# Kernel optimization log

Hardware: AMD Instinct MI355X
Metric: run time of the kernel (lower is better)

Reference implementation:

```python
import jax, jax.numpy as jnp
import numpy as np

# Each of the 16 binary logic ops (probabilistic relaxation) is affine in (1, a, b, a*b):
# op(a,b) = c0 + ca*a + cb*b + cab*a*b. Rows indexed by op id 0..15.
COEF = jnp.array([
    [0, 0, 0, 0],   # 0: false
    [0, 0, 0, 1],   # 1: a AND b
    [0, 1, 0, -1],  # 2: a AND NOT b
    [0, 1, 0, 0],   # 3: a
    [0, 0, 1, -1],  # 4: NOT a AND b
    [0, 0, 1, 0],   # 5: b
    [0, 1, 1, -2],  # 6: a XOR b
    [0, 1, 1, -1],  # 7: a OR b
    [1, -1, -1, 1], # 8: NOR
    [1, -1, -1, 2], # 9: XNOR
    [1, 0, -1, 0],  # 10: NOT b
    [1, 0, -1, 1],  # 11: a OR NOT b
    [1, -1, 0, 0],  # 12: NOT a
    [1, -1, 0, 1],  # 13: NOT a OR b
    [1, 0, 0, -1],  # 14: NAND
    [1, 0, 0, 0],   # 15: true
], dtype=jnp.float32)

B, C, H, W = 64, 32, 32, 32
K = 64            # num_kernels
D = 4             # tree_depth
S = 2 ** D        # sample_size = 16
RF, STRIDE, PAD = 5, 1, 0


def _make_indices(rng):
    # Replicates get_kernel_indices: per-kernel random (h,w,c) offsets, tiled over all
    # spatial positions. Returns a_idx, b_idx: [K, P, S, 3] with (h, w, c).
    h_starts = np.arange(0, H + 2 * PAD - RF + 1, STRIDE)
    w_starts = np.arange(0, W + 2 * PAD - RF + 1, STRIDE)
    hg, wg = np.meshgrid(h_starts, w_starts, indexing='ij')
    hg, wg = hg.ravel(), wg.ravel()           # [P]
    a_all, b_all = [], []
    for _ in range(K):
        h_off = rng.integers(0, RF, 2 * S)
        w_off = rng.integers(0, RF, 2 * S)
        c_off = rng.integers(0, C, 2 * S)
        hh = h_off[None, :] + hg[:, None]     # [P, 2S]
        ww = w_off[None, :] + wg[:, None]
        cc = np.broadcast_to(c_off[None, :], hh.shape)
        idx = np.stack([hh, ww, cc], axis=-1) # [P, 2S, 3]
        a_all.append(idx[:, :S])
        b_all.append(idx[:, S:])
    return np.stack(a_all).astype(np.int32), np.stack(b_all).astype(np.int32)


def setup_inputs() -> dict:
    key = jax.random.key(0)
    kx, k0, k1, k2, k3, k4 = jax.random.split(key, 6)
    rng = np.random.default_rng(0)
    a_idx, b_idx = _make_indices(rng)
    return {
        'x': jax.random.uniform(kx, (B, C, H, W), dtype=jnp.float32),
        'w0': jax.random.normal(k0, (16, K, 16), dtype=jnp.float32),
        'w1': jax.random.normal(k1, (8, K, 16), dtype=jnp.float32),
        'w2': jax.random.normal(k2, (4, K, 16), dtype=jnp.float32),
        'w3': jax.random.normal(k3, (2, K, 16), dtype=jnp.float32),
        'w4': jax.random.normal(k4, (1, K, 16), dtype=jnp.float32),
        'a_idx': jnp.asarray(a_idx),
        'b_idx': jnp.asarray(b_idx),
    }


def _bin_op(a, b, w):
    # a, b: [B, K, P, L]; w: [L, K, 16] raw logits (softmaxed per original).
    p = jax.nn.softmax(w, axis=-1)                 # [L, K, 16]
    coef = jnp.einsum('lko,oc->ckl', p, COEF)      # [4, K, L]
    c = coef[:, None, :, None, :]                  # [4, 1, K, 1, L]
    return c[0] + c[1] * a + c[2] * b + c[3] * (a * b)


def reference(x, w0, w1, w2, w3, w4, a_idx, b_idx):
    ah, aw, ac = a_idx[..., 0], a_idx[..., 1], a_idx[..., 2]
    bh, bw, bc = b_idx[..., 0], b_idx[..., 1], b_idx[..., 2]
    a = x[:, ac, ah, aw]    # [B, K, P, S]
    b = x[:, bc, bh, bw]
    cur = _bin_op(a, b, w0)
    for w in (w1, w2, w3, w4):
        cur = _bin_op(cur[..., 0::2], cur[..., 1::2], w)
    return cur              # [B, K, P, 1]
```

## Files before the change

kernel.cpp:

```cpp
#include <hip/hip_runtime.h>
#include <hip/hip_bf16.h>


#define B_  64
#define C_  32
#define H_  32
#define W_  32
#define K_  64
#define P_  784
#define CHW (C_*H_*W_)
#define HW  (H_*W_)
#define SITES (K_*P_)
#define NPAIR (P_/2)

__constant__ float COEF_[16][4] = {
    {0, 0, 0, 0}, {0, 0, 0, 1}, {0, 1, 0, -1}, {0, 1, 0, 0},
    {0, 0, 1, -1}, {0, 0, 1, 0}, {0, 1, 1, -2}, {0, 1, 1, -1},
    {1, -1, -1, 1}, {1, -1, -1, 2}, {1, 0, -1, 0}, {1, 0, -1, 1},
    {1, -1, 0, 0}, {1, -1, 0, 1}, {1, 0, 0, -1}, {1, 0, 0, 0}
};

__global__ __launch_bounds__(256) void prep_kernel(
    const int* __restrict__ a_idx, const int* __restrict__ b_idx,
    const float* __restrict__ w0, const float* __restrict__ w1,
    const float* __restrict__ w2, const float* __restrict__ w3,
    const float* __restrict__ w4,
    int* __restrict__ baseAB,
    float4* __restrict__ cws)
{
    const int t = blockIdx.x * 256 + threadIdx.x;
    if (t < K_ * 32) {
        const int k = t >> 5;
        const int j = t & 31;
        const int* src = (j < 16) ? a_idx : b_idx;
        const int l = j & 15;
        const size_t ii = ((size_t)k * P_ * 16 + l) * 3;
        const int h = src[ii + 0];
        const int w = src[ii + 1];
        const int c = src[ii + 2];
        baseAB[t] = (c << 12) + (h << 7) + (w << 2);
    } else if (t < K_ * 32 + K_ * 31) {
        const int tt = t - K_ * 32;
        const int k = tt / 31;
        const int node = tt - k * 31;
        int d, l;
        if      (node < 16) { d = 0; l = node; }
        else if (node < 24) { d = 1; l = node - 16; }
        else if (node < 28) { d = 2; l = node - 24; }
        else if (node < 30) { d = 3; l = node - 28; }
        else                { d = 4; l = 0; }
        const float* W;
        switch (d) {
            case 0: W = w0; break;
            case 1: W = w1; break;
            case 2: W = w2; break;
            case 3: W = w3; break;
            default: W = w4; break;
        }
        const float* row = W + ((size_t)l * K_ + k) * 16;
        float m = row[0];
        #pragma unroll
        for (int o = 1; o < 16; ++o) m = fmaxf(m, row[o]);
        float e[16];
        float Z = 0.0f;
        #pragma unroll
        for (int o = 0; o < 16; ++o) { e[o] = expf(row[o] - m); Z += e[o]; }
        const float inv = 1.0f / Z;
        float c0 = 0.f, c1 = 0.f, c2 = 0.f, c3 = 0.f;
        #pragma unroll
        for (int o = 0; o < 16; ++o) {
            c0 += e[o] * COEF_[o][0];
            c1 += e[o] * COEF_[o][1];
            c2 += e[o] * COEF_[o][2];
            c3 += e[o] * COEF_[o][3];
        }
        cws[tt] = make_float4(c0 * inv, c1 * inv, c2 * inv, c3 * inv);
    }
}

__device__ __forceinline__ float binop(float a, float b, float4 c) {
    return fmaf(b, fmaf(c.w, a, c.z), fmaf(c.y, a, c.x));
}

__global__ __launch_bounds__(1024, 4) void logicconv_main(
    const float* __restrict__ x,
    const int* __restrict__ baseAB,
    const float4* __restrict__ cws,
    float* __restrict__ out)
{
    __shared__ float simg[CHW];

    const int tid = threadIdx.x;
    const int kg  = blockIdx.x >> 5;
    const int bp  = blockIdx.x & 31;
    const int b0  = bp * 2;

    {
        const float4* xi = (const float4*)(x + (size_t)b0 * CHW);
        float4* si = (float4*)simg;
        #pragma unroll
        for (int j = 0; j < 8; ++j)
            si[tid + j * 1024] = xi[tid + j * 1024];
    }
    __syncthreads();

    const int g    = __builtin_amdgcn_readfirstlane(tid >> 7);
    const int lane = tid & 127;
    const int k    = kg * 8 + g;

    const int*    __restrict__ bA = baseAB + k * 32;
    const float4* __restrict__ cw = cws + (size_t)k * 31;
    const char*   sb = (const char*)simg;
    const char*   x1 = (const char*)(x + (size_t)(b0 + 1) * CHW);
    float* __restrict__ o0 = out + ((size_t)b0 * K_ + k) * P_;
    float* __restrict__ o1 = o0 + (size_t)K_ * P_;

    for (int s = 0; s < 4; ++s) {
        const int t = s * 128 + lane;
        if (t >= NPAIR) break;
        const unsigned row  = (unsigned)t / 14u;
        const unsigned disp = 8u * (unsigned)t + 16u * row;

        float2 ye[16], yo[16];
        #pragma unroll
        for (int l = 0; l < 16; ++l) {
            const unsigned ea = (unsigned)bA[l]      + disp;
            const unsigned eb = (unsigned)bA[16 + l] + disp;
            const float ae0 = *(const float*)(sb + ea);
            const float ae1 = *(const float*)(sb + ea + 4);
            const float be0 = *(const float*)(sb + eb);
            const float be1 = *(const float*)(sb + eb + 4);
            const float ao0 = *(const float*)(x1 + ea);
            const float ao1 = *(const float*)(x1 + ea + 4);
            const float bo0 = *(const float*)(x1 + eb);
            const float bo1 = *(const float*)(x1 + eb + 4);
            const float4 c = cw[l];
            ye[l].x = binop(ae0, be0, c);  ye[l].y = binop(ae1, be1, c);
            yo[l].x = binop(ao0, bo0, c);  yo[l].y = binop(ao1, bo1, c);
        }
        #pragma unroll
        for (int l = 0; l < 8; ++l) {
            const float4 c = cw[16 + l];
            ye[l].x = binop(ye[2*l].x, ye[2*l+1].x, c);
            ye[l].y = binop(ye[2*l].y, ye[2*l+1].y, c);
            yo[l].x = binop(yo[2*l].x, yo[2*l+1].x, c);
            yo[l].y = binop(yo[2*l].y, yo[2*l+1].y, c);
        }
        #pragma unroll
        for (int l = 0; l < 4; ++l) {
            const float4 c = cw[24 + l];
            ye[l].x = binop(ye[2*l].x, ye[2*l+1].x, c);
            ye[l].y = binop(ye[2*l].y, ye[2*l+1].y, c);
            yo[l].x = binop(yo[2*l].x, yo[2*l+1].x, c);
            yo[l].y = binop(yo[2*l].y, yo[2*l+1].y, c);
        }
        #pragma unroll
        for (int l = 0; l < 2; ++l) {
            const float4 c = cw[28 + l];
            ye[l].x = binop(ye[2*l].x, ye[2*l+1].x, c);
            ye[l].y = binop(ye[2*l].y, ye[2*l+1].y, c);
            yo[l].x = binop(yo[2*l].x, yo[2*l+1].x, c);
            yo[l].y = binop(yo[2*l].y, yo[2*l+1].y, c);
        }
        {
            const float4 c = cw[30];
            float2 re, ro;
            re.x = binop(ye[0].x, ye[1].x, c);
            re.y = binop(ye[0].y, ye[1].y, c);
            ro.x = binop(yo[0].x, yo[1].x, c);
            ro.y = binop(yo[0].y, yo[1].y, c);
            *(float2*)(o0 + 2 * t) = re;
            *(float2*)(o1 + 2 * t) = ro;
        }
    }
}

extern "C" void kernel_launch(void* const* d_in, const int* in_sizes, int n_in,
                              void* d_out, int out_size, void* d_ws, size_t ws_size,
                              hipStream_t stream) {
    const float* x     = (const float*)d_in[0];
    const float* w0    = (const float*)d_in[1];
    const float* w1    = (const float*)d_in[2];
    const float* w2    = (const float*)d_in[3];
    const float* w3    = (const float*)d_in[4];
    const float* w4    = (const float*)d_in[5];
    const int*   a_idx = (const int*)d_in[6];
    const int*   b_idx = (const int*)d_in[7];
    float* out = (float*)d_out;

    int*    baseAB = (int*)d_ws;
    float4* cws    = (float4*)((char*)d_ws + (size_t)K_ * 32 * 4);

    prep_kernel<<<16, 256, 0, stream>>>(a_idx, b_idx, w0, w1, w2, w3, w4,
                                        baseAB, cws);

    logicconv_main<<<256, 1024, 0, stream>>>(x, baseAB, cws, out);
}
```

Baseline: 32.31 us.

## Software-pipeline global gathers for odd batch behind LDS evaluation

```diff
diff --git a/kernel.cpp b/kernel.cpp
--- a/kernel.cpp
+++ b/kernel.cpp
@@ -95,15 +95,6 @@
     const int bp  = blockIdx.x & 31;
     const int b0  = bp * 2;
 
-    {
-        const float4* xi = (const float4*)(x + (size_t)b0 * CHW);
-        float4* si = (float4*)simg;
-        #pragma unroll
-        for (int j = 0; j < 8; ++j)
-            si[tid + j * 1024] = xi[tid + j * 1024];
-    }
-    __syncthreads();
-
     const int g    = __builtin_amdgcn_readfirstlane(tid >> 7);
     const int lane = tid & 127;
     const int k    = kg * 8 + g;
@@ -115,64 +106,120 @@
     float* __restrict__ o0 = out + ((size_t)b0 * K_ + k) * P_;
     float* __restrict__ o1 = o0 + (size_t)K_ * P_;
 
+    unsigned disp[4];
+    #pragma unroll
     for (int s = 0; s < 4; ++s) {
-        const int t = s * 128 + lane;
-        if (t >= NPAIR) break;
-        const unsigned row  = (unsigned)t / 14u;
-        const unsigned disp = 8u * (unsigned)t + 16u * row;
-
-        float2 ye[16], yo[16];
-        #pragma unroll
-        for (int l = 0; l < 16; ++l) {
-            const unsigned ea = (unsigned)bA[l]      + disp;
-            const unsigned eb = (unsigned)bA[16 + l] + disp;
-            const float ae0 = *(const float*)(sb + ea);
-            const float ae1 = *(const float*)(sb + ea + 4);
-            const float be0 = *(const float*)(sb + eb);
-            const float be1 = *(const float*)(sb + eb + 4);
-            const float ao0 = *(const float*)(x1 + ea);
-            const float ao1 = *(const float*)(x1 + ea + 4);
-            const float bo0 = *(const float*)(x1 + eb);
-            const float bo1 = *(const float*)(x1 + eb + 4);
-            const float4 c = cw[l];
-            ye[l].x = binop(ae0, be0, c);  ye[l].y = binop(ae1, be1, c);
-            yo[l].x = binop(ao0, bo0, c);  yo[l].y = binop(ao1, bo1, c);
-        }
-        #pragma unroll
-        for (int l = 0; l < 8; ++l) {
-            const float4 c = cw[16 + l];
-            ye[l].x = binop(ye[2*l].x, ye[2*l+1].x, c);
-            ye[l].y = binop(ye[2*l].y, ye[2*l+1].y, c);
-            yo[l].x = binop(yo[2*l].x, yo[2*l+1].x, c);
-            yo[l].y = binop(yo[2*l].y, yo[2*l+1].y, c);
-        }
-        #pragma unroll
-        for (int l = 0; l < 4; ++l) {
-            const float4 c = cw[24 + l];
-            ye[l].x = binop(ye[2*l].x, ye[2*l+1].x, c);
-            ye[l].y = binop(ye[2*l].y, ye[2*l+1].y, c);
-            yo[l].x = binop(yo[2*l].x, yo[2*l+1].x, c);
-            yo[l].y = binop(yo[2*l].y, yo[2*l+1].y, c);
-        }
-        #pragma unroll
-        for (int l = 0; l < 2; ++l) {
-            const float4 c = cw[28 + l];
-            ye[l].x = binop(ye[2*l].x, ye[2*l+1].x, c);
-            ye[l].y = binop(ye[2*l].y, ye[2*l+1].y, c);
-            yo[l].x = binop(yo[2*l].x, yo[2*l+1].x, c);
-            yo[l].y = binop(yo[2*l].y, yo[2*l+1].y, c);
-        }
-        {
-            const float4 c = cw[30];
-            float2 re, ro;
-            re.x = binop(ye[0].x, ye[1].x, c);
-            re.y = binop(ye[0].y, ye[1].y, c);
-            ro.x = binop(yo[0].x, yo[1].x, c);
-            ro.y = binop(yo[0].y, yo[1].y, c);
-            *(float2*)(o0 + 2 * t) = re;
-            *(float2*)(o1 + 2 * t) = ro;
-        }
+        unsigned t = s * 128 + lane;
+        if (t > NPAIR - 1) t = NPAIR - 1;
+        disp[s] = 8u * t + 16u * (t / 14u);
     }
+
+    float odA[32], odB[32];
+    float2 y1e[8], y1o[8];
+
+    #define ODLOAD(dst, hh, ss)                                        \
+        _Pragma("unroll")                                              \
+        for (int j = 0; j < 8; ++j) {                                  \
+            const int l = (hh) * 8 + j;                                \
+            const unsigned ga = (unsigned)bA[l]      + disp[ss];       \
+            const unsigned gb = (unsigned)bA[16 + l] + disp[ss];       \
+            dst[4*j+0] = *(const float*)(x1 + ga);                     \
+            dst[4*j+1] = *(const float*)(x1 + ga + 4);                 \
+            dst[4*j+2] = *(const float*)(x1 + gb);                     \
+            dst[4*j+3] = *(const float*)(x1 + gb + 4);                 \
+        }
+
+    #define EVL0L1(od, hh, ss)                                             \
+        _Pragma("unroll")                                                  \
+        for (int q = 0; q < 2; ++q) {                                      \
+            float ev[16];                                                  \
+            _Pragma("unroll")                                              \
+            for (int j = 0; j < 4; ++j) {                                  \
+                const int l = (hh) * 8 + q * 4 + j;                        \
+                const unsigned la = (unsigned)bA[l]      + disp[ss];       \
+                const unsigned lb = (unsigned)bA[16 + l] + disp[ss];       \
+                ev[4*j+0] = *(const float*)(sb + la);                      \
+                ev[4*j+1] = *(const float*)(sb + la + 4);                  \
+                ev[4*j+2] = *(const float*)(sb + lb);                      \
+                ev[4*j+3] = *(const float*)(sb + lb + 4);                  \
+            }                                                              \
+            _Pragma("unroll")                                              \
+            for (int j = 0; j < 2; ++j) {                                  \
+                const int l0 = (hh) * 8 + q * 4 + 2 * j;                   \
+                const int n1 = (hh) * 4 + q * 2 + j;      \
+                const float4 c0 = cw[l0], c1 = cw[l0 + 1];                 \
+                const float4 cL = cw[16 + n1];                             \
+                const int e0i = 8 * j, o0i = 16 * q + 8 * j;               \
+                float e0x = binop(ev[e0i+0], ev[e0i+2], c0);               \
+                float e0y = binop(ev[e0i+1], ev[e0i+3], c0);               \
+                float e1x = binop(ev[e0i+4], ev[e0i+6], c1);               \
+                float e1y = binop(ev[e0i+5], ev[e0i+7], c1);               \
+                float q0x = binop(od[o0i+0], od[o0i+2], c0);               \
+                float q0y = binop(od[o0i+1], od[o0i+3], c0);               \
+                float q1x = binop(od[o0i+4], od[o0i+6], c1);               \
+                float q1y = binop(od[o0i+5], od[o0i+7], c1);               \
+                y1e[n1].x = binop(e0x, e1x, cL);                           \
+                y1e[n1].y = binop(e0y, e1y, cL);                           \
+                y1o[n1].x = binop(q0x, q1x, cL);                           \
+                y1o[n1].y = binop(q0y, q1y, cL);                           \
+            }                                                              \
+        }
+
+    #define FINISH(ss)                                                     \
+        {                                                                  \
+            float2 y2e[4], y2o[4];                                         \
+            _Pragma("unroll")                                              \
+            for (int l = 0; l < 4; ++l) {                                  \
+                const float4 c = cw[24 + l];                               \
+                y2e[l].x = binop(y1e[2*l].x, y1e[2*l+1].x, c);             \
+                y2e[l].y = binop(y1e[2*l].y, y1e[2*l+1].y, c);             \
+                y2o[l].x = binop(y1o[2*l].x, y1o[2*l+1].x, c);             \
+                y2o[l].y = binop(y1o[2*l].y, y1o[2*l+1].y, c);             \
+            }                                                              \
+            float2 y3e[2], y3o[2];                                         \
+            _Pragma("unroll")                                              \
+            for (int l = 0; l < 2; ++l) {                                  \
+                const float4 c = cw[28 + l];                               \
+                y3e[l].x = binop(y2e[2*l].x, y2e[2*l+1].x, c);             \
+                y3e[l].y = binop(y2e[2*l].y, y2e[2*l+1].y, c);             \
+                y3o[l].x = binop(y2o[2*l].x, y2o[2*l+1].x, c);             \
+                y3o[l].y = binop(y2o[2*l].y, y2o[2*l+1].y, c);             \
+            }                                                              \
+            const float4 c4 = cw[30];                                      \
+            float2 re, ro;                                                 \
+            re.x = binop(y3e[0].x, y3e[1].x, c4);                          \
+            re.y = binop(y3e[0].y, y3e[1].y, c4);                          \
+            ro.x = binop(y3o[0].x, y3o[1].x, c4);                          \
+            ro.y = binop(y3o[0].y, y3o[1].y, c4);                          \
+            const int tt = (ss) * 128 + lane;                              \
+            if (tt < NPAIR) {                                              \
+                *(float2*)(o0 + 2 * tt) = re;                              \
+                *(float2*)(o1 + 2 * tt) = ro;                              \
+            }                                                              \
+        }
+
+    ODLOAD(odA, 0, 0)
+    {
+        const float4* xi = (const float4*)(x + (size_t)b0 * CHW);
+        float4* si = (float4*)simg;
+        #pragma unroll
+        for (int j = 0; j < 8; ++j)
+            si[tid + j * 1024] = xi[tid + j * 1024];
+    }
+    __syncthreads();
+
+    ODLOAD(odB, 1, 0)  EVL0L1(odA, 0, 0)
+    ODLOAD(odA, 0, 1)  EVL0L1(odB, 1, 0)  FINISH(0)
+    ODLOAD(odB, 1, 1)  EVL0L1(odA, 0, 1)
+    ODLOAD(odA, 0, 2)  EVL0L1(odB, 1, 1)  FINISH(1)
+    ODLOAD(odB, 1, 2)  EVL0L1(odA, 0, 2)
+    ODLOAD(odA, 0, 3)  EVL0L1(odB, 1, 2)  FINISH(2)
+    ODLOAD(odB, 1, 3)  EVL0L1(odA, 0, 3)
+                       EVL0L1(odB, 1, 3)  FINISH(3)
+
+    #undef ODLOAD
+    #undef EVL0L1
+    #undef FINISH
 }
 
 extern "C" void kernel_launch(void* const* d_in, const int* in_sizes, int n_in,
```

Result: slower. 33.36 us (+3.2%).

## Tile image rows into LDS with interleaved batch pairs and vector loads

Applied to the files above, without the earlier changes.

```diff
diff --git a/kernel.cpp b/kernel.cpp
--- a/kernel.cpp
+++ b/kernel.cpp
@@ -11,7 +11,10 @@
 #define CHW (C_*H_*W_)
 #define HW  (H_*W_)
 #define SITES (K_*P_)
-#define NPAIR (P_/2)
+#define NPAIRH 196
+#define NROWS 18
+#define TILEF (C_*NROWS*W_)
+#define LDSF  (2*TILEF)
 
 __constant__ float COEF_[16][4] = {
     {0, 0, 0, 0}, {0, 0, 0, 1}, {0, 1, 0, -1}, {0, 1, 0, 0},
@@ -20,12 +23,14 @@
     {1, -1, 0, 0}, {1, -1, 0, 1}, {1, 0, 0, -1}, {1, 0, 0, 0}
 };
 
+typedef float f4u __attribute__((ext_vector_type(4), aligned(8)));
+
 __global__ __launch_bounds__(256) void prep_kernel(
     const int* __restrict__ a_idx, const int* __restrict__ b_idx,
     const float* __restrict__ w0, const float* __restrict__ w1,
     const float* __restrict__ w2, const float* __restrict__ w3,
     const float* __restrict__ w4,
-    int* __restrict__ baseAB,
+    int* __restrict__ baseI,
     float4* __restrict__ cws)
 {
     const int t = blockIdx.x * 256 + threadIdx.x;
@@ -38,7 +43,7 @@
         const int h = src[ii + 0];
         const int w = src[ii + 1];
         const int c = src[ii + 2];
-        baseAB[t] = (c << 12) + (h << 7) + (w << 2);
+        baseI[t] = (c * 576 + h * 32 + w) * 8;
     } else if (t < K_ * 32 + K_ * 31) {
         const int tt = t - K_ * 32;
         const int k = tt / 31;
@@ -84,93 +89,111 @@
 
 __global__ __launch_bounds__(1024, 4) void logicconv_main(
     const float* __restrict__ x,
-    const int* __restrict__ baseAB,
+    const int* __restrict__ baseI,
     const float4* __restrict__ cws,
     float* __restrict__ out)
 {
-    __shared__ float simg[CHW];
+    __shared__ float simg[LDSF];
 
     const int tid = threadIdx.x;
-    const int kg  = blockIdx.x >> 5;
-    const int bp  = blockIdx.x & 31;
+    const int bid = blockIdx.x;
+    const int bp  = bid & 31;
+    const int ph  = (bid >> 5) & 1;
+    const int kq  = bid >> 6;
     const int b0  = bp * 2;
+    const int rlo = 14 * ph;
 
     {
-        const float4* xi = (const float4*)(x + (size_t)b0 * CHW);
-        float4* si = (float4*)simg;
-        #pragma unroll
-        for (int j = 0; j < 8; ++j)
-            si[tid + j * 1024] = xi[tid + j * 1024];
+        const char* xe = (const char*)(x + (size_t)b0 * CHW) + rlo * 128;
+        const char* xo = xe + (size_t)CHW * 4;
+        float4* sd = (float4*)simg;
+        #pragma unroll
+        for (int it = 0; it < 9; ++it) {
+            const int u  = it * 1024 + tid;
+            const int c  = u / 288;
+            const int rr = u - c * 288;
+            const int go = c * 4096 + rr * 8;
+            const float2 e = *(const float2*)(xe + go);
+            const float2 o = *(const float2*)(xo + go);
+            sd[u] = make_float4(e.x, o.x, e.y, o.y);
+        }
     }
     __syncthreads();
 
-    const int g    = __builtin_amdgcn_readfirstlane(tid >> 7);
-    const int lane = tid & 127;
-    const int k    = kg * 8 + g;
-
-    const int*    __restrict__ bA = baseAB + k * 32;
+    const int g    = __builtin_amdgcn_readfirstlane(tid >> 6);
+    const int lane = tid & 63;
+    const int k    = kq * 16 + g;
+
+    const int*    __restrict__ bI = baseI + k * 32;
     const float4* __restrict__ cw = cws + (size_t)k * 31;
     const char*   sb = (const char*)simg;
-    const char*   x1 = (const char*)(x + (size_t)(b0 + 1) * CHW);
-    float* __restrict__ o0 = out + ((size_t)b0 * K_ + k) * P_;
+    float* __restrict__ o0 = out + ((size_t)b0 * K_ + k) * P_ + 392 * ph;
     float* __restrict__ o1 = o0 + (size_t)K_ * P_;
 
     for (int s = 0; s < 4; ++s) {
-        const int t = s * 128 + lane;
-        if (t >= NPAIR) break;
-        const unsigned row  = (unsigned)t / 14u;
-        const unsigned disp = 8u * (unsigned)t + 16u * row;
-
-        float2 ye[16], yo[16];
-        #pragma unroll
-        for (int l = 0; l < 16; ++l) {
-            const unsigned ea = (unsigned)bA[l]      + disp;
-            const unsigned eb = (unsigned)bA[16 + l] + disp;
-            const float ae0 = *(const float*)(sb + ea);
-            const float ae1 = *(const float*)(sb + ea + 4);
-            const float be0 = *(const float*)(sb + eb);
-            const float be1 = *(const float*)(sb + eb + 4);
-            const float ao0 = *(const float*)(x1 + ea);
-            const float ao1 = *(const float*)(x1 + ea + 4);
-            const float bo0 = *(const float*)(x1 + eb);
-            const float bo1 = *(const float*)(x1 + eb + 4);
-            const float4 c = cw[l];
-            ye[l].x = binop(ae0, be0, c);  ye[l].y = binop(ae1, be1, c);
-            yo[l].x = binop(ao0, bo0, c);  yo[l].y = binop(ao1, bo1, c);
-        }
-        #pragma unroll
-        for (int l = 0; l < 8; ++l) {
-            const float4 c = cw[16 + l];
-            ye[l].x = binop(ye[2*l].x, ye[2*l+1].x, c);
-            ye[l].y = binop(ye[2*l].y, ye[2*l+1].y, c);
-            yo[l].x = binop(yo[2*l].x, yo[2*l+1].x, c);
-            yo[l].y = binop(yo[2*l].y, yo[2*l+1].y, c);
-        }
-        #pragma unroll
-        for (int l = 0; l < 4; ++l) {
-            const float4 c = cw[24 + l];
-            ye[l].x = binop(ye[2*l].x, ye[2*l+1].x, c);
-            ye[l].y = binop(ye[2*l].y, ye[2*l+1].y, c);
-            yo[l].x = binop(yo[2*l].x, yo[2*l+1].x, c);
-            yo[l].y = binop(yo[2*l].y, yo[2*l+1].y, c);
-        }
-        #pragma unroll
-        for (int l = 0; l < 2; ++l) {
-            const float4 c = cw[28 + l];
-            ye[l].x = binop(ye[2*l].x, ye[2*l+1].x, c);
-            ye[l].y = binop(ye[2*l].y, ye[2*l+1].y, c);
-            yo[l].x = binop(yo[2*l].x, yo[2*l+1].x, c);
-            yo[l].y = binop(yo[2*l].y, yo[2*l+1].y, c);
-        }
-        {
-            const float4 c = cw[30];
-            float2 re, ro;
-            re.x = binop(ye[0].x, ye[1].x, c);
-            re.y = binop(ye[0].y, ye[1].y, c);
-            ro.x = binop(yo[0].x, yo[1].x, c);
-            ro.y = binop(yo[0].y, yo[1].y, c);
-            *(float2*)(o0 + 2 * t) = re;
-            *(float2*)(o1 + 2 * t) = ro;
+        const int t = s * 64 + lane;
+        if (t < NPAIRH) {
+            const unsigned disp = 16u * (unsigned)t + 32u * ((unsigned)t / 14u);
+
+            float2 y1e[8], y1o[8];
+            #pragma unroll
+            for (int q = 0; q < 4; ++q) {
+                f4u rA[4], rB[4];
+                #pragma unroll
+                for (int j = 0; j < 4; ++j) {
+                    const int l = q * 4 + j;
+                    rA[j] = *(const f4u*)(sb + ((unsigned)bI[l]      + disp));
+                    rB[j] = *(const f4u*)(sb + ((unsigned)bI[16 + l] + disp));
+                }
+                #pragma unroll
+                for (int j = 0; j < 2; ++j) {
+                    const int jj = 2 * j;
+                    const float4 cA = cw[q * 4 + jj];
+                    const float4 cB = cw[q * 4 + jj + 1];
+                    const int n = q * 2 + j;
+                    const float4 cL = cw[16 + n];
+                    const float eL0 = binop(rA[jj].x,   rB[jj].x,   cA);
+                    const float oL0 = binop(rA[jj].y,   rB[jj].y,   cA);
+                    const float eH0 = binop(rA[jj].z,   rB[jj].z,   cA);
+                    const float oH0 = binop(rA[jj].w,   rB[jj].w,   cA);
+                    const float eL1 = binop(rA[jj+1].x, rB[jj+1].x, cB);
+                    const float oL1 = binop(rA[jj+1].y, rB[jj+1].y, cB);
+                    const float eH1 = binop(rA[jj+1].z, rB[jj+1].z, cB);
+                    const float oH1 = binop(rA[jj+1].w, rB[jj+1].w, cB);
+                    y1e[n].x = binop(eL0, eL1, cL);
+                    y1e[n].y = binop(eH0, eH1, cL);
+                    y1o[n].x = binop(oL0, oL1, cL);
+                    y1o[n].y = binop(oH0, oH1, cL);
+                }
+            }
+            float2 y2e[4], y2o[4];
+            #pragma unroll
+            for (int l = 0; l < 4; ++l) {
+                const float4 c = cw[24 + l];
+                y2e[l].x = binop(y1e[2*l].x, y1e[2*l+1].x, c);
+                y2e[l].y = binop(y1e[2*l].y, y1e[2*l+1].y, c);
+                y2o[l].x = binop(y1o[2*l].x, y1o[2*l+1].x, c);
+                y2o[l].y = binop(y1o[2*l].y, y1o[2*l+1].y, c);
+            }
+            float2 y3e[2], y3o[2];
+            #pragma unroll
+            for (int l = 0; l < 2; ++l) {
+                const float4 c = cw[28 + l];
+                y3e[l].x = binop(y2e[2*l].x, y2e[2*l+1].x, c);
+                y3e[l].y = binop(y2e[2*l].y, y2e[2*l+1].y, c);
+                y3o[l].x = binop(y2o[2*l].x, y2o[2*l+1].x, c);
+                y3o[l].y = binop(y2o[2*l].y, y2o[2*l+1].y, c);
+            }
+            {
+                const float4 c = cw[30];
+                float2 re, ro;
+                re.x = binop(y3e[0].x, y3e[1].x, c);
+                re.y = binop(y3e[0].y, y3e[1].y, c);
+                ro.x = binop(y3o[0].x, y3o[1].x, c);
+                ro.y = binop(y3o[0].y, y3o[1].y, c);
+                *(float2*)(o0 + 2 * t) = re;
+                *(float2*)(o1 + 2 * t) = ro;
+            }
         }
     }
 }
@@ -188,11 +211,11 @@
     const int*   b_idx = (const int*)d_in[7];
     float* out = (float*)d_out;
 
-    int*    baseAB = (int*)d_ws;
-    float4* cws    = (float4*)((char*)d_ws + (size_t)K_ * 32 * 4);
+    int*    baseI = (int*)d_ws;
+    float4* cws   = (float4*)((char*)d_ws + (size_t)K_ * 32 * 4);
 
     prep_kernel<<<16, 256, 0, stream>>>(a_idx, b_idx, w0, w1, w2, w3, w4,
-                                        baseAB, cws);
-
-    logicconv_main<<<256, 1024, 0, stream>>>(x, baseAB, cws, out);
-}
+                                        baseI, cws);
+
+    logicconv_main<<<256, 1024, 0, stream>>>(x, baseI, cws, out);
+}
```

Result: slower. 33.98 us (+5.2%).
